# Performance work log

Hardware: AMD Instinct MI355X
Metric: run time of the kernel (lower is better)

## Reference

```python
import jax, jax.numpy as jnp
import numpy as np

H = 8
D = 64  # head_dim = node_dim // num_heads = 512 // 8
NODE = 512
EPS = 1e-5


def setup_inputs() -> dict:
    key = jax.random.key(0)
    ks = jax.random.split(key, 8)
    S, IN = 4096, 1024
    return {
        "protT5_emb": jax.random.normal(ks[0], (S, IN), jnp.float32),
        "contact_matrix": jax.random.uniform(ks[1], (S, S), jnp.float32),
        "Wq": jax.random.normal(ks[2], (NODE, IN), jnp.float32) * 0.02,
        "bq": jnp.zeros((NODE,), jnp.float32),
        "Wk": jax.random.normal(ks[3], (NODE, IN), jnp.float32) * 0.02,
        "bk": jnp.zeros((NODE,), jnp.float32),
        "Wv": jax.random.normal(ks[4], (NODE, IN), jnp.float32) * 0.02,
        "bv": jnp.zeros((NODE,), jnp.float32),
        "Wc": jnp.ones((1, H, 1, 1), jnp.float32),
        "Wo": jax.random.normal(ks[5], (NODE, NODE), jnp.float32) * 0.02,
        "bo": jnp.zeros((NODE,), jnp.float32),
        "gamma": jnp.ones((NODE,), jnp.float32),
        "beta": jnp.zeros((NODE,), jnp.float32),
    }


def reference(protT5_emb, contact_matrix, Wq, bq, Wk, bk, Wv, bv, Wc, Wo, bo, gamma, beta):
    S = protT5_emb.shape[0]
    # QKV projections -> [H, S, D]
    Q = (protT5_emb @ Wq.T + bq).reshape(S, H, D).transpose(1, 0, 2)
    K = (protT5_emb @ Wk.T + bk).reshape(S, H, D).transpose(1, 0, 2)
    V = (protT5_emb @ Wv.T + bv).reshape(S, H, D).transpose(1, 0, 2)
    # raw scores [H, S, S]
    attn_raw = jnp.einsum('hsd,htd->hst', Q, K) / jnp.sqrt(jnp.float32(D))
    # multiplicative contact mask, per-head learnable scale
    contact_mask = contact_matrix[None, :, :] * Wc.reshape(H, 1, 1)
    attn_weight = jax.nn.softmax(attn_raw * contact_mask, axis=-1)
    attn_output = jnp.einsum('hst,htd->hsd', attn_weight, V)  # [H, S, D]
    # FAITHFUL to torch: transpose(0,1).view(S,-1) on [1,H,S,D] flattens in
    # (head, seq, dim) order -> scrambled [S, H*D] reshape, not head concat.
    attn_output = attn_output.reshape(S, H * D)
    aug = attn_output @ Wo.T + bo
    x = aug + protT5_emb[:, :NODE]
    mu = jnp.mean(x, axis=-1, keepdims=True)
    var = jnp.mean((x - mu) ** 2, axis=-1, keepdims=True)
    return (x - mu) * jax.lax.rsqrt(var + EPS) * gamma + beta
```

## Files before the change

kernel.cpp:

```cpp
#include <hip/hip_runtime.h>
#include <stdint.h>

#define SEQ 4096
#define INDIM 1024
#define NODEDIM 512
#define NH 8
#define HD 64
#define LSTR 72

typedef __bf16 bf16x8 __attribute__((ext_vector_type(8)));
typedef float f32x4 __attribute__((ext_vector_type(4)));

#define GLOAD_LDS(gp, lp) \
    __builtin_amdgcn_global_load_lds( \
        (const __attribute__((address_space(1))) void*)(gp), \
        (__attribute__((address_space(3))) void*)(lp), 16, 0, 0)

__device__ __forceinline__ unsigned short f2bf(float f) {
    union { float f; uint32_t u; } v; v.f = f;
    uint32_t u = v.u;
    uint32_t r = (u + 0x7fffu + ((u >> 16) & 1u)) >> 16;
    return (unsigned short)r;
}

__device__ __forceinline__ float fast_exp2(float x) {
    float r;
    asm volatile("v_exp_f32 %0, %1" : "=v"(r) : "v"(x));
    return r;
}

__global__ __launch_bounds__(256) void cvt_all(const float* __restrict__ emb,
                                               const float* __restrict__ Wq,
                                               const float* __restrict__ Wk,
                                               const float* __restrict__ Wv,
                                               const float* __restrict__ Wo,
                                               unsigned short* __restrict__ demb,
                                               unsigned short* __restrict__ dwqkv,
                                               unsigned short* __restrict__ dwo) {
    int b = blockIdx.x;
    const float* src;
    unsigned short* dst;
    int off;
    if (b < 4096)      { src = emb; dst = demb;            off = b; }
    else if (b < 4608) { src = Wq;  dst = dwqkv;           off = b - 4096; }
    else if (b < 5120) { src = Wk;  dst = dwqkv + 524288;  off = b - 4608; }
    else if (b < 5632) { src = Wv;  dst = dwqkv + 1048576; off = b - 5120; }
    else               { src = Wo;  dst = dwo;             off = b - 5632; }
    int i = (off * 256 + threadIdx.x) * 4;
    float4 v = *(const float4*)(src + i);
    ushort4 o;
    o.x = f2bf(v.x); o.y = f2bf(v.y); o.z = f2bf(v.z); o.w = f2bf(v.w);
    *(ushort4*)(dst + i) = o;
}

__global__ __launch_bounds__(256) void qkv_gemm(const unsigned short* __restrict__ A,
                                                const unsigned short* __restrict__ B,
                                                const float* __restrict__ bq,
                                                const float* __restrict__ bk,
                                                const float* __restrict__ bv,
                                                unsigned short* __restrict__ Qo,
                                                unsigned short* __restrict__ Ko,
                                                unsigned short* __restrict__ VTo) {
    __shared__ unsigned short As[128 * 32];
    __shared__ unsigned short Bs[128 * 32];
    __shared__ unsigned short Ts[128 * 40];
    const int tid = threadIdx.x;
    const int lane = tid & 63, wave = tid >> 6;
    const int wm = wave >> 1, wn = wave & 1;
    const int quad = lane >> 4, l16 = lane & 15;
    const int m0 = blockIdx.x * 128;
    const int n0 = blockIdx.y * 128;

    const int srow = tid >> 2, sqq = tid & 3;

    f32x4 acc[4][4] = {};

    for (int k0 = 0; k0 < INDIM; k0 += 32) {
        __syncthreads();
        for (int i = 0; i < 2; ++i) {
            int row = srow + 64 * i;
            GLOAD_LDS(A + (size_t)(m0 + row) * INDIM + k0 + sqq * 8, &As[row * 32 + sqq * 8]);
            GLOAD_LDS(B + (size_t)(n0 + row) * INDIM + k0 + sqq * 8, &Bs[row * 32 + sqq * 8]);
        }
        __syncthreads();
        bf16x8 af[4], bf[4];
        for (int mi = 0; mi < 4; ++mi)
            af[mi] = *(const bf16x8*)&As[(wm * 64 + mi * 16 + l16) * 32 + quad * 8];
        for (int ni = 0; ni < 4; ++ni)
            bf[ni] = *(const bf16x8*)&Bs[(wn * 64 + ni * 16 + l16) * 32 + quad * 8];
        for (int mi = 0; mi < 4; ++mi)
            for (int ni = 0; ni < 4; ++ni)
                acc[mi][ni] = __builtin_amdgcn_mfma_f32_16x16x32_bf16(af[mi], bf[ni], acc[mi][ni], 0, 0, 0);
    }

    if (blockIdx.y < 8) {
        unsigned short* outp = (blockIdx.y < 4) ? Qo : Ko;
        const float* biasp = (blockIdx.y < 4) ? bq : bk;
        for (int mi = 0; mi < 4; ++mi)
            for (int ni = 0; ni < 4; ++ni)
                for (int r = 0; r < 4; ++r) {
                    int s = m0 + wm * 64 + mi * 16 + quad * 4 + r;
                    int n = n0 + wn * 64 + ni * 16 + l16;
                    int h = (n >> 6) & 7;
                    int dd = n & 63;
                    float v = acc[mi][ni][r] + biasp[n & 511];
                    outp[((size_t)h * SEQ + s) * HD + dd] = f2bf(v);
                }
    } else {
        for (int chunk = 0; chunk < 4; ++chunk) {
            const int cwm = chunk >> 1;
            const int milo = (chunk & 1) * 2;
            __syncthreads();
            if (wm == cwm) {
                for (int mi2 = 0; mi2 < 2; ++mi2) {
                    int mi = milo + mi2;
                    for (int ni = 0; ni < 4; ++ni) {
                        int ddf = wn * 64 + ni * 16 + l16;
                        float bias = bv[(n0 + ddf) & 511];
                        for (int r = 0; r < 4; ++r) {
                            int sl = mi2 * 16 + quad * 4 + r;
                            Ts[ddf * 40 + sl] = f2bf(acc[mi][ni][r] + bias);
                        }
                    }
                }
            }
            __syncthreads();
            for (int pass = 0; pass < 2; ++pass) {
                int c = pass * 256 + tid;
                int row = c >> 2, part = c & 3;
                int nfull = n0 + row;
                int h = (nfull >> 6) & 7, dd = nfull & 63;
                *(bf16x8*)(VTo + ((size_t)h * HD + dd) * SEQ + m0 + chunk * 32 + part * 8) =
                    *(const bf16x8*)&Ts[row * 40 + part * 8];
            }
        }
    }
}

__global__ __launch_bounds__(256, 2) void attn_kernel(const unsigned short* __restrict__ Q,
                                                      const unsigned short* __restrict__ K,
                                                      const unsigned short* __restrict__ VT,
                                                      const float* __restrict__ CM,
                                                      const float* __restrict__ Wc,
                                                      float* __restrict__ O0,
                                                      float* __restrict__ O1,
                                                      float* __restrict__ l0,
                                                      float* __restrict__ l1) {
    __shared__ unsigned short QPs[128 * LSTR];
    __shared__ unsigned short Ks[64 * LSTR];
    __shared__ unsigned short Vs[64 * LSTR];
    const int tid = threadIdx.x;
    const int lane = tid & 63, wave = tid >> 6;
    const int quad = lane >> 4, l16 = lane & 15;
    const int h = blockIdx.y;
    const int q0 = blockIdx.x * 128;
    const int split = blockIdx.z;
    float* __restrict__ Op = split ? O1 : O0;
    float* __restrict__ lp = split ? l1 : l0;
    const float wch = Wc[h] * 0.125f * 1.44269504f;

    for (int i = 0; i < 4; ++i) {
        int c = tid + 256 * i;
        int row = c >> 3, part = c & 7;
        bf16x8 v = *(const bf16x8*)(Q + ((size_t)h * SEQ + q0 + row) * HD + part * 8);
        for (int j = 0; j < 8; ++j) v[j] = (__bf16)((float)v[j] * wch);
        *(bf16x8*)&QPs[row * LSTR + part * 8] = v;
    }

    const int tbeg = split * (SEQ / 2);
    const int tend = tbeg + SEQ / 2;

    const int srow0 = tid >> 3, spart = tid & 7;
    const int srow1 = (tid + 256) >> 3;
    const unsigned short* kp0 = K + ((size_t)h * SEQ + tbeg + srow0) * HD + spart * 8;
    const unsigned short* kp1 = K + ((size_t)h * SEQ + tbeg + srow1) * HD + spart * 8;
    const unsigned short* vp0 = VT + ((size_t)h * HD + srow0) * SEQ + tbeg + spart * 8;
    const unsigned short* vp1 = VT + ((size_t)h * HD + srow1) * SEQ + tbeg + spart * 8;
    bf16x8 kr0 = *(const bf16x8*)kp0;
    bf16x8 kr1 = *(const bf16x8*)kp1;
    bf16x8 vr0 = *(const bf16x8*)vp0;
    bf16x8 vr1 = *(const bf16x8*)vp1;

    __syncthreads();
    bf16x8 a[2][2];
    for (int mi = 0; mi < 2; ++mi) {
        a[mi][0] = *(const bf16x8*)&QPs[(wave * 32 + mi * 16 + l16) * LSTR + quad * 8];
        a[mi][1] = *(const bf16x8*)&QPs[(wave * 32 + mi * 16 + l16) * LSTR + 32 + quad * 8];
    }

    f32x4 O[2][4] = {};
    float l_part[2][4] = {};
    const float* cmbase0 = CM + (size_t)(q0 + wave * 32 + quad * 4) * SEQ + l16;
    const float* cmbase1 = cmbase0 + (size_t)16 * SEQ;

    for (int t0 = tbeg; t0 < tend; t0 += 64) {
        float cmv[2][4][4];
        for (int r = 0; r < 4; ++r)
            for (int nt = 0; nt < 4; ++nt) {
                cmv[0][r][nt] = cmbase0[(size_t)r * SEQ + t0 + nt * 16];
                cmv[1][r][nt] = cmbase1[(size_t)r * SEQ + t0 + nt * 16];
            }

        __syncthreads();
        *(bf16x8*)&Ks[srow0 * LSTR + spart * 8] = kr0;
        *(bf16x8*)&Ks[srow1 * LSTR + spart * 8] = kr1;
        *(bf16x8*)&Vs[srow0 * LSTR + spart * 8] = vr0;
        *(bf16x8*)&Vs[srow1 * LSTR + spart * 8] = vr1;
        __syncthreads();

        if (t0 + 64 < tend) {
            kr0 = *(const bf16x8*)(kp0 + (size_t)(t0 + 64 - tbeg) * HD);
            kr1 = *(const bf16x8*)(kp1 + (size_t)(t0 + 64 - tbeg) * HD);
            vr0 = *(const bf16x8*)(vp0 + (t0 + 64 - tbeg));
            vr1 = *(const bf16x8*)(vp1 + (t0 + 64 - tbeg));
        }

        f32x4 sc[2][4];
        for (int nt = 0; nt < 4; ++nt) {
            bf16x8 b0 = *(const bf16x8*)&Ks[(nt * 16 + l16) * LSTR + quad * 8];
            bf16x8 b1 = *(const bf16x8*)&Ks[(nt * 16 + l16) * LSTR + 32 + quad * 8];
            for (int mi = 0; mi < 2; ++mi) {
                f32x4 z = {0.f, 0.f, 0.f, 0.f};
                z = __builtin_amdgcn_mfma_f32_16x16x32_bf16(a[mi][0], b0, z, 0, 0, 0);
                z = __builtin_amdgcn_mfma_f32_16x16x32_bf16(a[mi][1], b1, z, 0, 0, 0);
                sc[mi][nt] = z;
            }
        }

        for (int mi = 0; mi < 2; ++mi)
            for (int r = 0; r < 4; ++r)
                for (int nt = 0; nt < 4; ++nt) {
                    float pv = fast_exp2(sc[mi][nt][r] * cmv[mi][r][nt]);
                    l_part[mi][r] += pv;
                    union { float f; uint32_t u; } pu; pu.f = pv;
                    QPs[(wave * 32 + mi * 16 + quad * 4 + r) * LSTR + nt * 16 + l16] =
                        (unsigned short)(pu.u >> 16);
                }

        asm volatile("s_waitcnt lgkmcnt(0)" ::: "memory");

        bf16x8 pa[2][2];
        for (int mi = 0; mi < 2; ++mi) {
            pa[mi][0] = *(const bf16x8*)&QPs[(wave * 32 + mi * 16 + l16) * LSTR + quad * 8];
            pa[mi][1] = *(const bf16x8*)&QPs[(wave * 32 + mi * 16 + l16) * LSTR + 32 + quad * 8];
        }
        for (int nt = 0; nt < 4; ++nt) {
            bf16x8 vb0 = *(const bf16x8*)&Vs[(nt * 16 + l16) * LSTR + quad * 8];
            bf16x8 vb1 = *(const bf16x8*)&Vs[(nt * 16 + l16) * LSTR + 32 + quad * 8];
            for (int mi = 0; mi < 2; ++mi) {
                f32x4 o = O[mi][nt];
                o = __builtin_amdgcn_mfma_f32_16x16x32_bf16(pa[mi][0], vb0, o, 0, 0, 0);
                o = __builtin_amdgcn_mfma_f32_16x16x32_bf16(pa[mi][1], vb1, o, 0, 0, 0);
                O[mi][nt] = o;
            }
        }
    }

    for (int mi = 0; mi < 2; ++mi)
        for (int r = 0; r < 4; ++r) {
            float s = l_part[mi][r];
            for (int off = 1; off < 16; off <<= 1) s += __shfl_xor(s, off);
            l_part[mi][r] = s;
        }
    if (l16 == 0)
        for (int mi = 0; mi < 2; ++mi)
            for (int r = 0; r < 4; ++r)
                lp[(size_t)h * SEQ + q0 + wave * 32 + mi * 16 + quad * 4 + r] = l_part[mi][r];
    for (int mi = 0; mi < 2; ++mi)
        for (int nt = 0; nt < 4; ++nt)
            for (int r = 0; r < 4; ++r) {
                int sg = q0 + wave * 32 + mi * 16 + quad * 4 + r;
                Op[((size_t)h * SEQ + sg) * HD + nt * 16 + l16] = O[mi][nt][r];
            }
}

__global__ __launch_bounds__(256) void combine_kernel(const float* __restrict__ O0,
                                                      const float* __restrict__ O1,
                                                      const float* __restrict__ l0,
                                                      const float* __restrict__ l1,
                                                      unsigned short* __restrict__ AO) {
    int idx = blockIdx.x * 256 + threadIdx.x;
    int e = idx * 4;
    int row = e >> 6;
    float4 a = *(const float4*)(O0 + e);
    float4 b = *(const float4*)(O1 + e);
    float linv = 1.f / (l0[row] + l1[row]);
    ushort4 o;
    o.x = f2bf((a.x + b.x) * linv);
    o.y = f2bf((a.y + b.y) * linv);
    o.z = f2bf((a.z + b.z) * linv);
    o.w = f2bf((a.w + b.w) * linv);
    *(ushort4*)(AO + e) = o;
}

__global__ __launch_bounds__(256) void out_gemm(const unsigned short* __restrict__ A,
                                                const unsigned short* __restrict__ B,
                                                const float* __restrict__ bo,
                                                const float* __restrict__ emb,
                                                float* __restrict__ X) {
    __shared__ unsigned short As[64 * 32];
    __shared__ unsigned short Bs[128 * 32];
    const int tid = threadIdx.x;
    const int lane = tid & 63, wave = tid >> 6;
    const int quad = lane >> 4, l16 = lane & 15;
    const int m0 = blockIdx.x * 64;
    const int n0 = blockIdx.y * 128;

    const int srow = tid >> 2, sqq = tid & 3;

    f32x4 acc[8] = {};

    for (int k0 = 0; k0 < NODEDIM; k0 += 32) {
        __syncthreads();
        GLOAD_LDS(A + (size_t)(m0 + srow) * NODEDIM + k0 + sqq * 8, &As[srow * 32 + sqq * 8]);
        for (int i = 0; i < 2; ++i) {
            int row = srow + 64 * i;
            GLOAD_LDS(B + (size_t)(n0 + row) * NODEDIM + k0 + sqq * 8, &Bs[row * 32 + sqq * 8]);
        }
        __syncthreads();
        bf16x8 af = *(const bf16x8*)&As[(wave * 16 + l16) * 32 + quad * 8];
        for (int ni = 0; ni < 8; ++ni) {
            bf16x8 bf = *(const bf16x8*)&Bs[(ni * 16 + l16) * 32 + quad * 8];
            acc[ni] = __builtin_amdgcn_mfma_f32_16x16x32_bf16(af, bf, acc[ni], 0, 0, 0);
        }
    }

    for (int ni = 0; ni < 8; ++ni)
        for (int r = 0; r < 4; ++r) {
            int s = m0 + wave * 16 + quad * 4 + r;
            int n = n0 + ni * 16 + l16;
            float v = acc[ni][r] + bo[n] + emb[(size_t)s * INDIM + n];
            X[(size_t)s * NODEDIM + n] = v;
        }
}

__global__ __launch_bounds__(256) void ln_kernel(const float* __restrict__ X,
                                                 const float* __restrict__ gamma,
                                                 const float* __restrict__ beta,
                                                 float* __restrict__ out) {
    const int s = blockIdx.x;
    const int n = threadIdx.x * 2;
    float2 v = *(const float2*)&X[(size_t)s * NODEDIM + n];
    float sum = v.x + v.y;
    float sq = v.x * v.x + v.y * v.y;
    for (int off = 32; off > 0; off >>= 1) {
        sum += __shfl_down(sum, off);
        sq += __shfl_down(sq, off);
    }
    __shared__ float ssum[4], ssq[4];
    const int wave = threadIdx.x >> 6, lane = threadIdx.x & 63;
    if (lane == 0) { ssum[wave] = sum; ssq[wave] = sq; }
    __syncthreads();
    float tsum = ssum[0] + ssum[1] + ssum[2] + ssum[3];
    float tsq = ssq[0] + ssq[1] + ssq[2] + ssq[3];
    float mu = tsum * (1.f / 512.f);
    float var = tsq * (1.f / 512.f) - mu * mu;
    float rstd = rsqrtf(var + 1e-5f);
    float2 g = *(const float2*)&gamma[n];
    float2 b = *(const float2*)&beta[n];
    float2 o;
    o.x = (v.x - mu) * rstd * g.x + b.x;
    o.y = (v.y - mu) * rstd * g.y + b.y;
    *(float2*)&out[(size_t)s * NODEDIM + n] = o;
}

extern "C" void kernel_launch(void* const* d_in, const int* in_sizes, int n_in,
                              void* d_out, int out_size, void* d_ws, size_t ws_size,
                              hipStream_t stream) {
    const float* emb = (const float*)d_in[0];
    const float* cm  = (const float*)d_in[1];
    const float* Wq  = (const float*)d_in[2];
    const float* bq  = (const float*)d_in[3];
    const float* Wk  = (const float*)d_in[4];
    const float* bk  = (const float*)d_in[5];
    const float* Wv  = (const float*)d_in[6];
    const float* bv  = (const float*)d_in[7];
    const float* Wc  = (const float*)d_in[8];
    const float* Wo  = (const float*)d_in[9];
    const float* bo  = (const float*)d_in[10];
    const float* gamma = (const float*)d_in[11];
    const float* beta  = (const float*)d_in[12];
    float* out = (float*)d_out;

    unsigned short* ws = (unsigned short*)d_ws;
    unsigned short* emb_bf  = ws;
    unsigned short* wqkv_bf = emb_bf + 4194304;
    unsigned short* wo_bf   = wqkv_bf + 1572864;
    unsigned short* Qb  = wo_bf + 262144;
    unsigned short* Kb  = Qb + 2097152;
    unsigned short* VTb = Kb + 2097152;
    unsigned short* AOb = VTb + 2097152;
    float* X = (float*)(AOb + 2097152);
    float* O0 = (float*)emb_bf;
    float* O1 = X;
    float* l0 = (float*)wqkv_bf;
    float* l1 = l0 + NH * SEQ;

    cvt_all<<<5888, 256, 0, stream>>>(emb, Wq, Wk, Wv, Wo, emb_bf, wqkv_bf, wo_bf);

    qkv_gemm<<<dim3(32, 12), 256, 0, stream>>>(emb_bf, wqkv_bf, bq, bk, bv, Qb, Kb, VTb);
    attn_kernel<<<dim3(32, 8, 2), 256, 0, stream>>>(Qb, Kb, VTb, cm, Wc, O0, O1, l0, l1);
    combine_kernel<<<2048, 256, 0, stream>>>(O0, O1, l0, l1, AOb);
    out_gemm<<<dim3(64, 4), 256, 0, stream>>>(AOb, wo_bf, bo, emb, X);
    ln_kernel<<<4096, 256, 0, stream>>>(X, gamma, beta, out);
}
```

Before: 256.5 us.

## Split attention key range four ways and swizzle P tile LDS layout

The attention kernel now splits the key dimension into four chunks instead of two when the workspace is large enough, giving 1024 blocks instead of 512. It also asks for four blocks per CU in launch bounds and XOR-swizzles the LDS layout of the probability tile to cut bank conflicts between the write and the MFMA operand read. The combine kernel adds the two extra partial outputs and row sums. The cost is more partial-output traffic, tighter register limits, and a dependence on workspace size for which path runs.

```diff
diff --git a/kernel.cpp b/kernel.cpp
--- a/kernel.cpp
+++ b/kernel.cpp
@@ -137,15 +137,20 @@
     }
 }
 
-__global__ __launch_bounds__(256, 2) void attn_kernel(const unsigned short* __restrict__ Q,
+__global__ __launch_bounds__(256, 4) void attn_kernel(const unsigned short* __restrict__ Q,
                                                       const unsigned short* __restrict__ K,
                                                       const unsigned short* __restrict__ VT,
                                                       const float* __restrict__ CM,
                                                       const float* __restrict__ Wc,
                                                       float* __restrict__ O0,
                                                       float* __restrict__ O1,
+                                                      float* __restrict__ O2,
+                                                      float* __restrict__ O3,
                                                       float* __restrict__ l0,
-                                                      float* __restrict__ l1) {
+                                                      float* __restrict__ l1,
+                                                      float* __restrict__ l2,
+                                                      float* __restrict__ l3,
+                                                      int tcount) {
     __shared__ unsigned short QPs[128 * LSTR];
     __shared__ unsigned short Ks[64 * LSTR];
     __shared__ unsigned short Vs[64 * LSTR];
@@ -155,8 +160,8 @@
     const int h = blockIdx.y;
     const int q0 = blockIdx.x * 128;
     const int split = blockIdx.z;
-    float* __restrict__ Op = split ? O1 : O0;
-    float* __restrict__ lp = split ? l1 : l0;
+    float* __restrict__ Op = (split == 0) ? O0 : (split == 1) ? O1 : (split == 2) ? O2 : O3;
+    float* __restrict__ lp = (split == 0) ? l0 : (split == 1) ? l1 : (split == 2) ? l2 : l3;
     const float wch = Wc[h] * 0.125f * 1.44269504f;
 
     for (int i = 0; i < 4; ++i) {
@@ -167,8 +172,8 @@
         *(bf16x8*)&QPs[row * LSTR + part * 8] = v;
     }
 
-    const int tbeg = split * (SEQ / 2);
-    const int tend = tbeg + SEQ / 2;
+    const int tbeg = split * tcount;
+    const int tend = tbeg + tcount;
 
     const int srow0 = tid >> 3, spart = tid & 7;
     const int srow1 = (tid + 256) >> 3;
@@ -192,6 +197,7 @@
     float l_part[2][4] = {};
     const float* cmbase0 = CM + (size_t)(q0 + wave * 32 + quad * 4) * SEQ + l16;
     const float* cmbase1 = cmbase0 + (size_t)16 * SEQ;
+    const int sw = (l16 >> 2) & 3;
 
     for (int t0 = tbeg; t0 < tend; t0 += 64) {
         float cmv[2][4][4];
@@ -233,7 +239,8 @@
                     float pv = fast_exp2(sc[mi][nt][r] * cmv[mi][r][nt]);
                     l_part[mi][r] += pv;
                     union { float f; uint32_t u; } pu; pu.f = pv;
-                    QPs[(wave * 32 + mi * 16 + quad * 4 + r) * LSTR + nt * 16 + l16] =
+                    QPs[(wave * 32 + mi * 16 + quad * 4 + r) * LSTR
+                        + (((nt * 2 + (l16 >> 3)) ^ quad) << 3) + (l16 & 7)] =
                         (unsigned short)(pu.u >> 16);
                 }
 
@@ -241,8 +248,8 @@
 
         bf16x8 pa[2][2];
         for (int mi = 0; mi < 2; ++mi) {
-            pa[mi][0] = *(const bf16x8*)&QPs[(wave * 32 + mi * 16 + l16) * LSTR + quad * 8];
-            pa[mi][1] = *(const bf16x8*)&QPs[(wave * 32 + mi * 16 + l16) * LSTR + 32 + quad * 8];
+            pa[mi][0] = *(const bf16x8*)&QPs[(wave * 32 + mi * 16 + l16) * LSTR + ((quad ^ sw) << 3)];
+            pa[mi][1] = *(const bf16x8*)&QPs[(wave * 32 + mi * 16 + l16) * LSTR + 32 + ((quad ^ sw) << 3)];
         }
         for (int nt = 0; nt < 4; ++nt) {
             bf16x8 vb0 = *(const bf16x8*)&Vs[(nt * 16 + l16) * LSTR + quad * 8];
@@ -276,20 +283,33 @@
 
 __global__ __launch_bounds__(256) void combine_kernel(const float* __restrict__ O0,
                                                       const float* __restrict__ O1,
+                                                      const float* __restrict__ O2,
+                                                      const float* __restrict__ O3,
                                                       const float* __restrict__ l0,
                                                       const float* __restrict__ l1,
+                                                      const float* __restrict__ l2,
+                                                      const float* __restrict__ l3,
+                                                      int nsplit,
                                                       unsigned short* __restrict__ AO) {
     int idx = blockIdx.x * 256 + threadIdx.x;
     int e = idx * 4;
     int row = e >> 6;
     float4 a = *(const float4*)(O0 + e);
     float4 b = *(const float4*)(O1 + e);
-    float linv = 1.f / (l0[row] + l1[row]);
+    float x = a.x + b.x, y = a.y + b.y, z = a.z + b.z, w = a.w + b.w;
+    float ls = l0[row] + l1[row];
+    if (nsplit == 4) {
+        float4 c = *(const float4*)(O2 + e);
+        float4 d = *(const float4*)(O3 + e);
+        x += c.x + d.x; y += c.y + d.y; z += c.z + d.z; w += c.w + d.w;
+        ls += l2[row] + l3[row];
+    }
+    float linv = 1.f / ls;
     ushort4 o;
-    o.x = f2bf((a.x + b.x) * linv);
-    o.y = f2bf((a.y + b.y) * linv);
-    o.z = f2bf((a.z + b.z) * linv);
-    o.w = f2bf((a.w + b.w) * linv);
+    o.x = f2bf(x * linv);
+    o.y = f2bf(y * linv);
+    o.z = f2bf(z * linv);
+    o.w = f2bf(w * linv);
     *(ushort4*)(AO + e) = o;
 }
 
@@ -393,14 +413,22 @@
     float* X = (float*)(AOb + 2097152);
     float* O0 = (float*)emb_bf;
     float* O1 = X;
+    float* O2 = X + 2097152;
+    float* O3 = O2 + 2097152;
     float* l0 = (float*)wqkv_bf;
     float* l1 = l0 + NH * SEQ;
+    float* l2 = l1 + NH * SEQ;
+    float* l3 = l2 + NH * SEQ;
+
+    const size_t NEED4 = 54001664ull;
+    const int nz = (ws_size >= NEED4) ? 4 : 2;
 
     cvt_all<<<5888, 256, 0, stream>>>(emb, Wq, Wk, Wv, Wo, emb_bf, wqkv_bf, wo_bf);
 
     qkv_gemm<<<dim3(32, 12), 256, 0, stream>>>(emb_bf, wqkv_bf, bq, bk, bv, Qb, Kb, VTb);
-    attn_kernel<<<dim3(32, 8, 2), 256, 0, stream>>>(Qb, Kb, VTb, cm, Wc, O0, O1, l0, l1);
-    combine_kernel<<<2048, 256, 0, stream>>>(O0, O1, l0, l1, AOb);
+    attn_kernel<<<dim3(32, 8, nz), 256, 0, stream>>>(Qb, Kb, VTb, cm, Wc,
+                                                     O0, O1, O2, O3, l0, l1, l2, l3, SEQ / nz);
+    combine_kernel<<<2048, 256, 0, stream>>>(O0, O1, O2, O3, l0, l1, l2, l3, nz, AOb);
     out_gemm<<<dim3(64, 4), 256, 0, stream>>>(AOb, wo_bf, bo, emb, X);
     ln_kernel<<<4096, 256, 0, stream>>>(X, gamma, beta, out);
 }
```

Measured after the change: 387.4 us. 1.51x slower.
